# Performance work log

Measured on AMD Instinct MI355X. Metric: run time of the kernel, lower is better.

The kernel has to match this reference:

```python
import jax, jax.numpy as jnp
import numpy as np
import math

B, S, HD, NH, L, FF = 8, 512, 768, 12, 12, 3072
DH = HD // NH
EPS = 1e-12
REL_BINS, MAX_REL = 32, 128
REL2D_BINS, MAX_REL2D = 64, 256


def rel_bucket(rel_pos, num_buckets, max_distance):
    # bidirectional bucketing, faithful to relative_position_bucket
    nb = num_buckets // 2
    ret = (rel_pos > 0).astype(jnp.int32) * nb
    n = jnp.abs(rel_pos).astype(jnp.int32)
    max_exact = nb // 2
    is_small = n < max_exact
    scale = (nb - max_exact) / math.log(max_distance / max_exact)
    val = max_exact + (jnp.log(jnp.maximum(n, 1).astype(jnp.float32) / max_exact) * scale).astype(jnp.int32)
    val = jnp.minimum(val, nb - 1)
    return ret + jnp.where(is_small, n, val)


def layernorm(x, g, b):
    m = jnp.mean(x, axis=-1, keepdims=True)
    v = jnp.var(x, axis=-1, keepdims=True)
    return (x - m) * jax.lax.rsqrt(v + EPS) * g + b


def setup_inputs() -> dict:
    key = jax.random.key(0)
    ks = jax.random.split(key, 12)
    r = lambda k, shape: jax.random.normal(k, shape, jnp.float32) * 0.02
    z = lambda shape: jnp.zeros(shape, jnp.float32)
    o = lambda shape: jnp.ones(shape, jnp.float32)
    return {
        'hidden_states': jax.random.normal(ks[0], (B, S, HD), jnp.float32),
        'attention_mask': jnp.zeros((B, 1, 1, S), jnp.bool_),  # True = masked
        'position_ids': jnp.broadcast_to(jnp.arange(S, dtype=jnp.int32), (B, S)),
        'bbox': jax.random.randint(ks[1], (B, S, 4), 0, 1000, dtype=jnp.int32),
        'qkv_w': r(ks[2], (L, HD, 3 * HD)),
        'q_bias': z((L, HD)), 'v_bias': z((L, HD)),
        'attn_out_w': r(ks[3], (L, HD, HD)), 'attn_out_b': z((L, HD)),
        'ln1_g': o((L, HD)), 'ln1_b': z((L, HD)),
        'inter_w': r(ks[4], (L, HD, FF)), 'inter_b': z((L, FF)),
        'out_w': r(ks[5], (L, FF, HD)), 'out_b': z((L, HD)),
        'ln2_g': o((L, HD)), 'ln2_b': z((L, HD)),
        'rel_pos_w': r(ks[6], (REL_BINS, NH)),
        'rel_x_w': r(ks[7], (REL2D_BINS, NH)),
        'rel_y_w': r(ks[8], (REL2D_BINS, NH)),
    }


def reference(hidden_states, attention_mask, position_ids, bbox,
              qkv_w, q_bias, v_bias, attn_out_w, attn_out_b, ln1_g, ln1_b,
              inter_w, inter_b, out_w, out_b, ln2_g, ln2_b,
              rel_pos_w, rel_x_w, rel_y_w):
    # ---- 1D relative position bias: [B, NH, S, S] ----
    rp = position_ids[:, None, :] - position_ids[:, :, None]  # mem - query
    rel_pos = rel_pos_w[rel_bucket(rp, REL_BINS, MAX_REL)]     # [B,S,S,NH]
    rel_pos = rel_pos.transpose(0, 3, 1, 2)
    # ---- 2D spatial bias from bbox x (col 0) and y (col 3) ----
    px, py = bbox[:, :, 0], bbox[:, :, 3]
    bx = rel_bucket(px[:, None, :] - px[:, :, None], REL2D_BINS, MAX_REL2D)
    by = rel_bucket(py[:, None, :] - py[:, :, None], REL2D_BINS, MAX_REL2D)
    rel_2d = (rel_x_w[bx] + rel_y_w[by]).transpose(0, 3, 1, 2)  # [B,NH,S,S]
    bias = rel_pos + rel_2d
    mask = attention_mask.astype(jnp.bool_)  # [B,1,1,S], True = masked
    inv_sqrt_dh = 1.0 / math.sqrt(DH)

    def heads(x):  # [B,S,HD] -> [B,NH,S,DH]
        return x.reshape(B, S, NH, DH).transpose(0, 2, 1, 3)

    def layer(h, p):
        qw, qb, vb, aow, aob, g1, b1, iw, ib, ow, ob, g2, b2 = p
        qkv = h @ qw  # fast_qkv, no bias on the fused linear
        q, k, v = jnp.split(qkv, 3, axis=-1)
        q = heads(q + qb) * inv_sqrt_dh
        k = heads(k)
        v = heads(v + vb)
        scores = jnp.einsum('bhsd,bhtd->bhst', q, k) + bias
        scores = jnp.where(mask, -jnp.inf, scores.astype(jnp.float32))
        probs = jax.nn.softmax(scores, axis=-1).astype(h.dtype)
        ctx = jnp.einsum('bhst,bhtd->bhsd', probs, v)
        ctx = ctx.transpose(0, 2, 1, 3).reshape(B, S, HD)
        attn = layernorm(ctx @ aow + aob + h, g1, b1)
        ffn = jax.nn.gelu(attn @ iw + ib, approximate=False)
        out = layernorm(ffn @ ow + ob + attn, g2, b2)
        return out, None

    params = (qkv_w, q_bias, v_bias, attn_out_w, attn_out_b, ln1_g, ln1_b,
              inter_w, inter_b, out_w, out_b, ln2_g, ln2_b)
    h, _ = jax.lax.scan(layer, hidden_states, params)
    return h
```

## Files before the change

### kernel.cpp

```cpp
#include <hip/hip_runtime.h>
#include <math.h>

typedef unsigned short u16;
typedef short bf16x8 __attribute__((ext_vector_type(8)));
typedef unsigned short u16x8 __attribute__((ext_vector_type(8)));
typedef float f32x4 __attribute__((ext_vector_type(4)));

#define L_  12
#define B_  8
#define S_  512
#define HD_ 768
#define NH_ 12
#define DH_ 64
#define FF_ 3072

__device__ __forceinline__ u16 f2bf(float f) {
    unsigned u = __float_as_uint(f);
    u += 0x7fffu + ((u >> 16) & 1u);
    return (u16)(u >> 16);
}
__device__ __forceinline__ float bf2f(u16 h) {
    return __uint_as_float(((unsigned)h) << 16);
}

__device__ __forceinline__ void ld_lds16(const u16* g, u16* l) {
    __builtin_amdgcn_global_load_lds((const __attribute__((address_space(1))) void*)g,
                                     (__attribute__((address_space(3))) void*)l, 16, 0, 0);
}

__device__ __forceinline__ int rel_bucket(int rel, int num_buckets, int max_distance) {
    int nb = num_buckets >> 1;
    int ret = (rel > 0) ? nb : 0;
    int n = abs(rel);
    int max_exact = nb >> 1;
    if (n < max_exact) return ret + n;
    float scale = (float)(nb - max_exact) / logf((float)max_distance / (float)max_exact);
    int val = max_exact + (int)(logf(fmaxf((float)n, 1.0f) / (float)max_exact) * scale);
    val = min(val, nb - 1);
    return ret + val;
}

__global__ __launch_bounds__(256) void transpose_k(const float* __restrict__ in,
                                                   u16* __restrict__ out, int K, int N) {
    __shared__ u16 tile[32][33];
    const int k0 = blockIdx.x * 32, n0 = blockIdx.y * 32;
    const int tx = threadIdx.x & 31, ty = threadIdx.x >> 5;
#pragma unroll
    for (int r = 0; r < 32; r += 8)
        tile[ty + r][tx] = f2bf(in[(long)(k0 + ty + r) * N + n0 + tx]);
    __syncthreads();
#pragma unroll
    for (int r = 0; r < 32; r += 8)
        out[(long)(n0 + ty + r) * K + k0 + tx] = tile[tx][ty + r];
}

__global__ __launch_bounds__(256) void bucket_k(const int* __restrict__ pos,
                                                const int* __restrict__ bbox,
                                                unsigned* __restrict__ out) {
    const int bi = blockIdx.x;
    const int b = bi >> 9;
    const int t = threadIdx.x;
    const int pos_i = pos[bi];
    const int px_i = bbox[bi * 4 + 0];
    const int py_i = bbox[bi * 4 + 3];
    for (int j = t; j < S_; j += 256) {
        int bp = rel_bucket(pos[b * S_ + j] - pos_i, 32, 128);
        int bx = rel_bucket(bbox[(b * S_ + j) * 4 + 0] - px_i, 64, 256);
        int by = rel_bucket(bbox[(b * S_ + j) * 4 + 3] - py_i, 64, 256);
        out[((long)bi << 9) + j] = (unsigned)bp | ((unsigned)bx << 8) | ((unsigned)by << 16);
    }
}

__global__ __launch_bounds__(256) void init_k(const float* __restrict__ hs,
                                              float* __restrict__ h, u16* __restrict__ hb) {
    const int i = blockIdx.x * 256 + threadIdx.x;
    float v = hs[i];
    h[i] = v;
    hb[i] = f2bf(v);
}

template <int EPI>
__global__ __launch_bounds__(256) void gemm128_k(
    const u16* __restrict__ A, const u16* __restrict__ Bt, int N, int K, int Kc,
    long zStride,
    const float* __restrict__ bias, const float* __restrict__ bias2,
    float* __restrict__ outF,
    u16* __restrict__ oB0, u16* __restrict__ oB1, u16* __restrict__ oB2) {
    __shared__ __align__(16) u16 As[128 * 32];
    __shared__ __align__(16) u16 Bs[128 * 32];
    const int tid = threadIdx.x;
    const int wave = tid >> 6, lane = tid & 63;
    const int lrow = lane & 15, quad = lane >> 4;
    const int wr = wave >> 1, wc = wave & 1;
    const long zoff = (long)blockIdx.z * Kc;
    const u16* Ag = A + (long)blockIdx.x * 128 * K + (long)(tid >> 2) * K + ((tid & 3) << 3) + zoff;
    const u16* Bg = Bt + (long)blockIdx.y * 128 * K + (long)(tid >> 2) * K + ((tid & 3) << 3) + zoff;
    const long rs64 = (long)64 * K;
    u16* Al = As + tid * 8;
    u16* Bl = Bs + tid * 8;
    f32x4 acc[4][4] = {};
    for (int k0 = 0; k0 < Kc; k0 += 32) {
        ld_lds16(Ag + k0, Al);
        ld_lds16(Ag + rs64 + k0, Al + 2048);
        ld_lds16(Bg + k0, Bl);
        ld_lds16(Bg + rs64 + k0, Bl + 2048);
        __syncthreads();
        bf16x8 a[4], b[4];
#pragma unroll
        for (int i = 0; i < 4; i++)
            a[i] = *(const bf16x8*)(As + (wr * 64 + i * 16 + lrow) * 32 + (quad << 3));
#pragma unroll
        for (int j = 0; j < 4; j++)
            b[j] = *(const bf16x8*)(Bs + (wc * 64 + j * 16 + lrow) * 32 + (quad << 3));
#pragma unroll
        for (int i = 0; i < 4; i++)
#pragma unroll
            for (int j = 0; j < 4; j++)
                acc[i][j] = __builtin_amdgcn_mfma_f32_16x16x32_bf16(a[i], b[j], acc[i][j], 0, 0, 0);
        __syncthreads();
    }
    const int rbase = blockIdx.x * 128 + wr * 64 + (quad << 2);
    const int cbase = blockIdx.y * 128 + wc * 64 + lrow;
    const bool addb = (blockIdx.z == 0);
#pragma unroll
    for (int i = 0; i < 4; i++) {
#pragma unroll
        for (int j = 0; j < 4; j++) {
            const int gc = cbase + j * 16;
#pragma unroll
            for (int r = 0; r < 4; r++) {
                const int gr = rbase + i * 16 + r;
                float v = acc[i][j][r];
                if (EPI == 0) {
                    if (addb) v += bias[gc];
                    outF[(long)blockIdx.z * zStride + (long)gr * N + gc] = v;
                } else if (EPI == 1) {
                    v += bias[gc];
                    v = 0.5f * v * (1.0f + erff(v * 0.70710678118654752f));
                    oB0[(long)gr * N + gc] = f2bf(v);
                } else {
                    int b = gr >> 9, s = gr & 511;
                    int part = gc / HD_;
                    int cm = gc - part * HD_;
                    int hh = cm >> 6, d = cm & 63;
                    long hb = (long)(b * NH_ + hh);
                    if (part == 0) {
                        float q = (v + bias[cm]) * 0.125f;
                        oB0[(hb * S_ + s) * DH_ + d] = f2bf(q);
                    } else if (part == 1) {
                        oB1[(hb * S_ + s) * DH_ + d] = f2bf(v);
                    } else {
                        oB2[(hb * DH_ + d) * S_ + s] = f2bf(v + bias2[cm]);
                    }
                }
            }
        }
    }
}

__global__ __launch_bounds__(256) void attn_fused_k(
    const u16* __restrict__ q, const u16* __restrict__ k, const u16* __restrict__ vt,
    const unsigned* __restrict__ bk,
    const float* __restrict__ rpw, const float* __restrict__ rxw,
    const float* __restrict__ ryw, u16* __restrict__ ctx) {
    __shared__ float tb[1920];
    __shared__ __align__(16) u16 P[32768];
    const int t = threadIdx.x;
    for (int i = t; i < 384; i += 256) tb[i] = rpw[i];
    for (int i = t; i < 768; i += 256) { tb[384 + i] = rxw[i]; tb[1152 + i] = ryw[i]; }
    const int wv = t >> 6, lane = t & 63;
    const int lrow = lane & 15, quad = lane >> 4;
    const int bh = blockIdx.y, b = bh / NH_, h = bh - b * NH_;
    const int qt = blockIdx.x;
    const int q0 = qt * 64 + wv * 16;
    const u16* qb = q + ((long)bh * S_ + q0 + lrow) * DH_ + (quad << 3);
    const u16* kb = k + ((long)bh * S_ + lrow) * DH_ + (quad << 3);
    bf16x8 aq0 = *(const bf16x8*)qb;
    bf16x8 aq1 = *(const bf16x8*)(qb + 32);
    __syncthreads();
    f32x4 acc[32];
#pragma unroll
    for (int ct = 0; ct < 32; ct++) {
        const u16* kp = kb + (long)(ct * 16) * DH_;
        bf16x8 b0 = *(const bf16x8*)kp;
        bf16x8 b1 = *(const bf16x8*)(kp + 32);
        f32x4 z = {0.f, 0.f, 0.f, 0.f};
        z = __builtin_amdgcn_mfma_f32_16x16x32_bf16(aq0, b0, z, 0, 0, 0);
        acc[ct] = __builtin_amdgcn_mfma_f32_16x16x32_bf16(aq1, b1, z, 0, 0, 0);
    }
    float mx[4] = {-1e30f, -1e30f, -1e30f, -1e30f};
    const unsigned* bkb = bk + ((long)(b * S_ + q0 + (quad << 2)) << 9) + lrow;
#pragma unroll
    for (int r = 0; r < 4; r++) {
        const unsigned* br = bkb + ((long)r << 9);
#pragma unroll
        for (int ct = 0; ct < 32; ct++) {
            unsigned kk = br[ct * 16];
            float bi = tb[(kk & 255) * 12 + h] + tb[384 + ((kk >> 8) & 255) * 12 + h]
                     + tb[1152 + ((kk >> 16) & 255) * 12 + h];
            float x = acc[ct][r] + bi;
            acc[ct][r] = x;
            mx[r] = fmaxf(mx[r], x);
        }
    }
#pragma unroll
    for (int r = 0; r < 4; r++)
#pragma unroll
        for (int o = 8; o > 0; o >>= 1) mx[r] = fmaxf(mx[r], __shfl_xor(mx[r], o));
    float sm[4] = {0.f, 0.f, 0.f, 0.f};
#pragma unroll
    for (int ct = 0; ct < 32; ct++) {
#pragma unroll
        for (int r = 0; r < 4; r++) {
            float e = __expf(acc[ct][r] - mx[r]);
            acc[ct][r] = e;
            sm[r] += e;
        }
    }
#pragma unroll
    for (int r = 0; r < 4; r++) {
#pragma unroll
        for (int o = 8; o > 0; o >>= 1) sm[r] += __shfl_xor(sm[r], o);
        sm[r] = 1.0f / sm[r];
    }
    const int prow_w = (wv << 4) + (quad << 2);
#pragma unroll
    for (int ct = 0; ct < 32; ct++) {
#pragma unroll
        for (int r = 0; r < 4; r++) {
            int row = prow_w + r;
            int col = ct * 16 + lrow;
            int off = (row << 10) + ((((col >> 3) ^ (row & 7)) << 4)) + ((col & 7) << 1);
            *(u16*)((char*)P + off) = f2bf(acc[ct][r] * sm[r]);
        }
    }
    __syncthreads();
    f32x4 o[4] = {};
    const u16* vb = vt + ((long)bh * DH_ + lrow) * S_ + (quad << 3);
    const int prow = (wv << 4) + lrow;
#pragma unroll
    for (int c = 0; c < 16; c++) {
        int col0 = c * 32 + (quad << 3);
        int aoff = (prow << 10) + ((((col0 >> 3) ^ (prow & 7)) << 4));
        bf16x8 ap = *(const bf16x8*)((char*)P + aoff);
#pragma unroll
        for (int dt = 0; dt < 4; dt++) {
            bf16x8 bv = *(const bf16x8*)(vb + (long)(dt * 16) * S_ + c * 32);
            o[dt] = __builtin_amdgcn_mfma_f32_16x16x32_bf16(ap, bv, o[dt], 0, 0, 0);
        }
    }
    u16* cb = ctx + ((long)(b * S_ + qt * 64 + (wv << 4) + (quad << 2))) * HD_ + h * DH_ + lrow;
#pragma unroll
    for (int dt = 0; dt < 4; dt++)
#pragma unroll
        for (int i = 0; i < 4; i++)
            cb[(long)i * HD_ + dt * 16] = f2bf(o[dt][i]);
}

__global__ __launch_bounds__(256) void ln_k(const float* __restrict__ x0,
                                            const float* __restrict__ x1,
                                            const float* __restrict__ res,
                                            const float* __restrict__ g,
                                            const float* __restrict__ b,
                                            float* __restrict__ outF,
                                            u16* __restrict__ outB) {
    const long row = blockIdx.x;
    const float* xr = x0 + row * HD_;
    const float* yr = x1 + row * HD_;
    const float* rr = res + row * HD_;
    const int t = threadIdx.x;
    float v0 = xr[t] + yr[t] + rr[t];
    float v1 = xr[t + 256] + yr[t + 256] + rr[t + 256];
    float v2 = xr[t + 512] + yr[t + 512] + rr[t + 512];
    __shared__ float red[256];
    red[t] = v0 + v1 + v2;
    __syncthreads();
    for (int o = 128; o > 0; o >>= 1) {
        if (t < o) red[t] += red[t + o];
        __syncthreads();
    }
    float mean = red[0] * (1.0f / 768.0f);
    __syncthreads();
    float d0 = v0 - mean, d1 = v1 - mean, d2 = v2 - mean;
    red[t] = d0 * d0 + d1 * d1 + d2 * d2;
    __syncthreads();
    for (int o = 128; o > 0; o >>= 1) {
        if (t < o) red[t] += red[t + o];
        __syncthreads();
    }
    float rstd = rsqrtf(red[0] * (1.0f / 768.0f) + 1e-12f);
    float y0 = d0 * rstd * g[t] + b[t];
    float y1 = d1 * rstd * g[t + 256] + b[t + 256];
    float y2 = d2 * rstd * g[t + 512] + b[t + 512];
    outF[row * HD_ + t] = y0;
    outF[row * HD_ + t + 256] = y1;
    outF[row * HD_ + t + 512] = y2;
    outB[row * HD_ + t] = f2bf(y0);
    outB[row * HD_ + t + 256] = f2bf(y1);
    outB[row * HD_ + t + 512] = f2bf(y2);
}

extern "C" void kernel_launch(void* const* d_in, const int* in_sizes, int n_in,
                              void* d_out, int out_size, void* d_ws, size_t ws_size,
                              hipStream_t stream) {
    const float* hs     = (const float*)d_in[0];
    const int*   pos    = (const int*)d_in[2];
    const int*   bbox   = (const int*)d_in[3];
    const float* qkv_w  = (const float*)d_in[4];
    const float* q_bias = (const float*)d_in[5];
    const float* v_bias = (const float*)d_in[6];
    const float* aow    = (const float*)d_in[7];
    const float* aob    = (const float*)d_in[8];
    const float* g1     = (const float*)d_in[9];
    const float* b1     = (const float*)d_in[10];
    const float* iw     = (const float*)d_in[11];
    const float* ib     = (const float*)d_in[12];
    const float* ow     = (const float*)d_in[13];
    const float* ob     = (const float*)d_in[14];
    const float* g2     = (const float*)d_in[15];
    const float* b2     = (const float*)d_in[16];
    const float* rpw    = (const float*)d_in[17];
    const float* rxw    = (const float*)d_in[18];
    const float* ryw    = (const float*)d_in[19];

    char* wp = (char*)d_ws;
    auto take = [&](size_t bytes) -> char* {
        char* p = wp;
        wp += (bytes + 255) & ~(size_t)255;
        return p;
    };
    u16*   wq     = (u16*)take((size_t)2304 * 768 * 2);
    u16*   wa     = (u16*)take((size_t)768 * 768 * 2);
    u16*   wiT    = (u16*)take((size_t)3072 * 768 * 2);
    u16*   woT    = (u16*)take((size_t)768 * 3072 * 2);
    unsigned* buckets = (unsigned*)take((size_t)B_ * S_ * S_ * 4);
    char*  regA   = take((size_t)B_ * NH_ * S_ * S_ * 2);
    float* tmpF   = (float*)regA;
    float* tmpF2  = (float*)(regA + (size_t)B_ * S_ * HD_ * 4);
    u16*   ffnb   = (u16*)(regA + (size_t)2 * B_ * S_ * HD_ * 4);
    u16*   qbuf   = (u16*)take((size_t)B_ * NH_ * S_ * DH_ * 2);
    u16*   kbuf   = (u16*)take((size_t)B_ * NH_ * S_ * DH_ * 2);
    u16*   vtbuf  = (u16*)take((size_t)B_ * NH_ * S_ * DH_ * 2);
    u16*   hbf    = (u16*)take((size_t)B_ * S_ * HD_ * 2);
    u16*   ctxb   = (u16*)take((size_t)B_ * S_ * HD_ * 2);
    float* attnF  = (float*)take((size_t)B_ * S_ * HD_ * 4);
    u16*   attnB  = (u16*)take((size_t)B_ * S_ * HD_ * 2);

    if ((size_t)(wp - (char*)d_ws) > ws_size) return;

    dim3 blk(256);
    float* hout = (float*)d_out;
    const long ZS = (long)4096 * 768;

    bucket_k<<<dim3(B_ * S_), blk, 0, stream>>>(pos, bbox, buckets);
    init_k<<<dim3((B_ * S_ * HD_) / 256), blk, 0, stream>>>(hs, hout, hbf);

    for (int l = 0; l < L_; l++) {
        transpose_k<<<dim3(24, 72), blk, 0, stream>>>(qkv_w + (size_t)l * 768 * 2304, wq, 768, 2304);
        transpose_k<<<dim3(24, 24), blk, 0, stream>>>(aow + (size_t)l * 768 * 768, wa, 768, 768);
        transpose_k<<<dim3(24, 96), blk, 0, stream>>>(iw + (size_t)l * 768 * 3072, wiT, 768, 3072);
        transpose_k<<<dim3(96, 24), blk, 0, stream>>>(ow + (size_t)l * 3072 * 768, woT, 3072, 768);

        gemm128_k<2><<<dim3(32, 18, 1), blk, 0, stream>>>(
            hbf, wq, 2304, 768, 768, 0L, q_bias + l * HD_, v_bias + l * HD_,
            nullptr, qbuf, kbuf, vtbuf);

        attn_fused_k<<<dim3(8, 96), blk, 0, stream>>>(qbuf, kbuf, vtbuf, buckets,
                                                      rpw, rxw, ryw, ctxb);

        gemm128_k<0><<<dim3(32, 6, 2), blk, 0, stream>>>(
            ctxb, wa, 768, 768, 384, ZS, aob + l * HD_, nullptr,
            tmpF, nullptr, nullptr, nullptr);

        ln_k<<<dim3(B_ * S_), blk, 0, stream>>>(tmpF, tmpF2, hout,
                                                g1 + l * HD_, b1 + l * HD_, attnF, attnB);

        gemm128_k<1><<<dim3(32, 24, 1), blk, 0, stream>>>(
            attnB, wiT, 3072, 768, 768, 0L, ib + l * FF_, nullptr,
            nullptr, ffnb, nullptr, nullptr);

        gemm128_k<0><<<dim3(32, 6, 2), blk, 0, stream>>>(
            ffnb, woT, 768, 3072, 1536, ZS, ob + l * HD_, nullptr,
            tmpF, nullptr, nullptr, nullptr);

        ln_k<<<dim3(B_ * S_), blk, 0, stream>>>(tmpF, tmpF2, attnF,
                                                g2 + l * HD_, b2 + l * HD_, hout, hbf);
    }
}
```

Before: 3.676 ms.

## Precompute bf16 relative-position bias once and restructure attention P staging

Adds a bias_k kernel that expands bucket indices into a per-head bf16 bias tensor once, before the layer loop, so each layer's attention reads bias directly instead of doing three LDS table lookups per score. The attention kernel now computes K·Q (transposed) so each lane holds one query row, which simplifies the max and sum reductions to two shuffles. It also replaces the 64KB shared P buffer with small per-wave 4KB chunks processed in four column slices, with launch_bounds(256,3) to raise occupancy. The cost is an extra ~50MB workspace buffer and higher memory traffic for reading bf16 bias in every layer, with a fallback path when the workspace is too small.

```diff
diff --git a/kernel.cpp b/kernel.cpp
--- a/kernel.cpp
+++ b/kernel.cpp
@@ -68,6 +68,28 @@
         int bx = rel_bucket(bbox[(b * S_ + j) * 4 + 0] - px_i, 64, 256);
         int by = rel_bucket(bbox[(b * S_ + j) * 4 + 3] - py_i, 64, 256);
         out[((long)bi << 9) + j] = (unsigned)bp | ((unsigned)bx << 8) | ((unsigned)by << 16);
+    }
+}
+
+__global__ __launch_bounds__(256) void bias_k(const unsigned* __restrict__ bk,
+                                              const float* __restrict__ rpw,
+                                              const float* __restrict__ rxw,
+                                              const float* __restrict__ ryw,
+                                              u16* __restrict__ out) {
+    __shared__ float tb[1920];
+    const int t = threadIdx.x;
+    for (int i = t; i < 384; i += 256) tb[i] = rpw[i];
+    for (int i = t; i < 768; i += 256) { tb[384 + i] = rxw[i]; tb[1152 + i] = ryw[i]; }
+    __syncthreads();
+    const int bi = blockIdx.x;
+    const int b = bi >> 9, i = bi & 511;
+    const unsigned* br = bk + ((long)bi << 9);
+    for (int idx = t; idx < NH_ * S_; idx += 256) {
+        const int h = idx >> 9, j = idx & 511;
+        unsigned kk = br[j];
+        float v = tb[(kk & 255) * 12 + h] + tb[384 + ((kk >> 8) & 255) * 12 + h] +
+                  tb[1152 + ((kk >> 16) & 255) * 12 + h];
+        out[((long)(b * NH_ + h) * S_ + i) * S_ + j] = f2bf(v);
     }
 }
 
@@ -158,16 +180,19 @@
     }
 }
 
-__global__ __launch_bounds__(256) void attn_fused_k(
+template <bool USEB>
+__global__ __launch_bounds__(256, 3) void attn_fused_k(
     const u16* __restrict__ q, const u16* __restrict__ k, const u16* __restrict__ vt,
-    const unsigned* __restrict__ bk,
+    const u16* __restrict__ bias, const unsigned* __restrict__ bk,
     const float* __restrict__ rpw, const float* __restrict__ rxw,
     const float* __restrict__ ryw, u16* __restrict__ ctx) {
     __shared__ float tb[1920];
-    __shared__ __align__(16) u16 P[32768];
+    __shared__ __align__(16) u16 Pw[4][2048];
     const int t = threadIdx.x;
-    for (int i = t; i < 384; i += 256) tb[i] = rpw[i];
-    for (int i = t; i < 768; i += 256) { tb[384 + i] = rxw[i]; tb[1152 + i] = ryw[i]; }
+    if constexpr (!USEB) {
+        for (int i = t; i < 384; i += 256) tb[i] = rpw[i];
+        for (int i = t; i < 768; i += 256) { tb[384 + i] = rxw[i]; tb[1152 + i] = ryw[i]; }
+    }
     const int wv = t >> 6, lane = t & 63;
     const int lrow = lane & 15, quad = lane >> 4;
     const int bh = blockIdx.y, b = bh / NH_, h = bh - b * NH_;
@@ -175,81 +200,97 @@
     const int q0 = qt * 64 + wv * 16;
     const u16* qb = q + ((long)bh * S_ + q0 + lrow) * DH_ + (quad << 3);
     const u16* kb = k + ((long)bh * S_ + lrow) * DH_ + (quad << 3);
-    bf16x8 aq0 = *(const bf16x8*)qb;
-    bf16x8 aq1 = *(const bf16x8*)(qb + 32);
-    __syncthreads();
+    bf16x8 qf0 = *(const bf16x8*)qb;
+    bf16x8 qf1 = *(const bf16x8*)(qb + 32);
+    if constexpr (!USEB) __syncthreads();
     f32x4 acc[32];
 #pragma unroll
     for (int ct = 0; ct < 32; ct++) {
         const u16* kp = kb + (long)(ct * 16) * DH_;
-        bf16x8 b0 = *(const bf16x8*)kp;
-        bf16x8 b1 = *(const bf16x8*)(kp + 32);
+        bf16x8 k0 = *(const bf16x8*)kp;
+        bf16x8 k1 = *(const bf16x8*)(kp + 32);
         f32x4 z = {0.f, 0.f, 0.f, 0.f};
-        z = __builtin_amdgcn_mfma_f32_16x16x32_bf16(aq0, b0, z, 0, 0, 0);
-        acc[ct] = __builtin_amdgcn_mfma_f32_16x16x32_bf16(aq1, b1, z, 0, 0, 0);
-    }
-    float mx[4] = {-1e30f, -1e30f, -1e30f, -1e30f};
-    const unsigned* bkb = bk + ((long)(b * S_ + q0 + (quad << 2)) << 9) + lrow;
-#pragma unroll
-    for (int r = 0; r < 4; r++) {
-        const unsigned* br = bkb + ((long)r << 9);
+        z = __builtin_amdgcn_mfma_f32_16x16x32_bf16(k0, qf0, z, 0, 0, 0);
+        acc[ct] = __builtin_amdgcn_mfma_f32_16x16x32_bf16(k1, qf1, z, 0, 0, 0);
+    }
+    float m = -1e30f;
+    if constexpr (USEB) {
+        const u16* bb = bias + ((long)bh * S_ + q0 + lrow) * S_ + (quad << 2);
 #pragma unroll
         for (int ct = 0; ct < 32; ct++) {
-            unsigned kk = br[ct * 16];
-            float bi = tb[(kk & 255) * 12 + h] + tb[384 + ((kk >> 8) & 255) * 12 + h]
-                     + tb[1152 + ((kk >> 16) & 255) * 12 + h];
-            float x = acc[ct][r] + bi;
-            acc[ct][r] = x;
-            mx[r] = fmaxf(mx[r], x);
-        }
-    }
-#pragma unroll
-    for (int r = 0; r < 4; r++)
-#pragma unroll
-        for (int o = 8; o > 0; o >>= 1) mx[r] = fmaxf(mx[r], __shfl_xor(mx[r], o));
-    float sm[4] = {0.f, 0.f, 0.f, 0.f};
+            ushort4 b4 = *(const ushort4*)(bb + ct * 16);
+            acc[ct][0] += bf2f(b4.x);
+            acc[ct][1] += bf2f(b4.y);
+            acc[ct][2] += bf2f(b4.z);
+            acc[ct][3] += bf2f(b4.w);
+            m = fmaxf(m, fmaxf(fmaxf(acc[ct][0], acc[ct][1]), fmaxf(acc[ct][2], acc[ct][3])));
+        }
+    } else {
+        const unsigned* br = bk + ((long)(b * S_ + q0 + lrow) << 9) + (quad << 2);
+#pragma unroll
+        for (int ct = 0; ct < 32; ct++) {
+            uint4 k4 = *(const uint4*)(br + ct * 16);
+            unsigned ka[4] = {k4.x, k4.y, k4.z, k4.w};
+#pragma unroll
+            for (int r = 0; r < 4; r++) {
+                unsigned kk = ka[r];
+                acc[ct][r] += tb[(kk & 255) * 12 + h] + tb[384 + ((kk >> 8) & 255) * 12 + h] +
+                              tb[1152 + ((kk >> 16) & 255) * 12 + h];
+            }
+            m = fmaxf(m, fmaxf(fmaxf(acc[ct][0], acc[ct][1]), fmaxf(acc[ct][2], acc[ct][3])));
+        }
+    }
+    m = fmaxf(m, __shfl_xor(m, 16));
+    m = fmaxf(m, __shfl_xor(m, 32));
+    float s = 0.f;
 #pragma unroll
     for (int ct = 0; ct < 32; ct++) {
 #pragma unroll
         for (int r = 0; r < 4; r++) {
-            float e = __expf(acc[ct][r] - mx[r]);
+            float e = __expf(acc[ct][r] - m);
             acc[ct][r] = e;
-            sm[r] += e;
-        }
-    }
-#pragma unroll
-    for (int r = 0; r < 4; r++) {
-#pragma unroll
-        for (int o = 8; o > 0; o >>= 1) sm[r] += __shfl_xor(sm[r], o);
-        sm[r] = 1.0f / sm[r];
-    }
-    const int prow_w = (wv << 4) + (quad << 2);
-#pragma unroll
-    for (int ct = 0; ct < 32; ct++) {
-#pragma unroll
-        for (int r = 0; r < 4; r++) {
-            int row = prow_w + r;
-            int col = ct * 16 + lrow;
-            int off = (row << 10) + ((((col >> 3) ^ (row & 7)) << 4)) + ((col & 7) << 1);
-            *(u16*)((char*)P + off) = f2bf(acc[ct][r] * sm[r]);
-        }
-    }
-    __syncthreads();
+            s += e;
+        }
+    }
+    s += __shfl_xor(s, 16);
+    s += __shfl_xor(s, 32);
+    const float inv = 1.0f / s;
     f32x4 o[4] = {};
     const u16* vb = vt + ((long)bh * DH_ + lrow) * S_ + (quad << 3);
-    const int prow = (wv << 4) + lrow;
-#pragma unroll
-    for (int c = 0; c < 16; c++) {
-        int col0 = c * 32 + (quad << 3);
-        int aoff = (prow << 10) + ((((col0 >> 3) ^ (prow & 7)) << 4));
-        bf16x8 ap = *(const bf16x8*)((char*)P + aoff);
-#pragma unroll
-        for (int dt = 0; dt < 4; dt++) {
-            bf16x8 bv = *(const bf16x8*)(vb + (long)(dt * 16) * S_ + c * 32);
-            o[dt] = __builtin_amdgcn_mfma_f32_16x16x32_bf16(ap, bv, o[dt], 0, 0, 0);
-        }
-    }
-    u16* cb = ctx + ((long)(b * S_ + qt * 64 + (wv << 4) + (quad << 2))) * HD_ + h * DH_ + lrow;
+    u16* pw = &Pw[wv][0];
+    const int wg = quad >> 1;
+    const int wbyte = (quad & 1) << 3;
+    const int rsw = lrow & 7;
+#pragma unroll
+    for (int c = 0; c < 4; c++) {
+        asm volatile("s_waitcnt lgkmcnt(0)" ::: "memory");
+        __builtin_amdgcn_sched_barrier(0);
+#pragma unroll
+        for (int lc = 0; lc < 8; lc++) {
+            const f32x4 a = acc[c * 8 + lc];
+            ushort4 pk;
+            pk.x = f2bf(a[0] * inv);
+            pk.y = f2bf(a[1] * inv);
+            pk.z = f2bf(a[2] * inv);
+            pk.w = f2bf(a[3] * inv);
+            const int g = lc * 2 + wg;
+            *(ushort4*)((char*)pw + lrow * 256 + (((g ^ rsw)) << 4) + wbyte) = pk;
+        }
+        asm volatile("s_waitcnt lgkmcnt(0)" ::: "memory");
+        __builtin_amdgcn_sched_barrier(0);
+#pragma unroll
+        for (int ss = 0; ss < 4; ss++) {
+            bf16x8 ap = *(const bf16x8*)((char*)pw + lrow * 256 +
+                                         ((((ss << 2) + quad) ^ rsw) << 4));
+            const u16* vp = vb + c * 128 + ss * 32;
+#pragma unroll
+            for (int dt = 0; dt < 4; dt++) {
+                bf16x8 bv = *(const bf16x8*)(vp + (long)(dt * 16) * S_);
+                o[dt] = __builtin_amdgcn_mfma_f32_16x16x32_bf16(ap, bv, o[dt], 0, 0, 0);
+            }
+        }
+    }
+    u16* cb = ctx + ((long)(b * S_ + qt * 64 + wv * 16 + (quad << 2))) * HD_ + h * DH_ + lrow;
 #pragma unroll
     for (int dt = 0; dt < 4; dt++)
 #pragma unroll
@@ -345,8 +386,11 @@
     u16*   ctxb   = (u16*)take((size_t)B_ * S_ * HD_ * 2);
     float* attnF  = (float*)take((size_t)B_ * S_ * HD_ * 4);
     u16*   attnB  = (u16*)take((size_t)B_ * S_ * HD_ * 2);
-
-    if ((size_t)(wp - (char*)d_ws) > ws_size) return;
+    char*  base_end = wp;
+    u16*   biasT  = (u16*)take((size_t)B_ * NH_ * S_ * S_ * 2);
+
+    if ((size_t)(base_end - (char*)d_ws) > ws_size) return;
+    const bool useBias = (size_t)(wp - (char*)d_ws) <= ws_size;
 
     dim3 blk(256);
     float* hout = (float*)d_out;
@@ -354,6 +398,8 @@
 
     bucket_k<<<dim3(B_ * S_), blk, 0, stream>>>(pos, bbox, buckets);
     init_k<<<dim3((B_ * S_ * HD_) / 256), blk, 0, stream>>>(hs, hout, hbf);
+    if (useBias)
+        bias_k<<<dim3(B_ * S_), blk, 0, stream>>>(buckets, rpw, rxw, ryw, biasT);
 
     for (int l = 0; l < L_; l++) {
         transpose_k<<<dim3(24, 72), blk, 0, stream>>>(qkv_w + (size_t)l * 768 * 2304, wq, 768, 2304);
@@ -365,8 +411,12 @@
             hbf, wq, 2304, 768, 768, 0L, q_bias + l * HD_, v_bias + l * HD_,
             nullptr, qbuf, kbuf, vtbuf);
 
-        attn_fused_k<<<dim3(8, 96), blk, 0, stream>>>(qbuf, kbuf, vtbuf, buckets,
-                                                      rpw, rxw, ryw, ctxb);
+        if (useBias)
+            attn_fused_k<true><<<dim3(8, 96), blk, 0, stream>>>(
+                qbuf, kbuf, vtbuf, biasT, buckets, rpw, rxw, ryw, ctxb);
+        else
+            attn_fused_k<false><<<dim3(8, 96), blk, 0, stream>>>(
+                qbuf, kbuf, vtbuf, nullptr, buckets, rpw, rxw, ryw, ctxb);
 
         gemm128_k<0><<<dim3(32, 6, 2), blk, 0, stream>>>(
             ctxb, wa, 768, 768, 384, ZS, aob + l * HD_, nullptr,
```

Result: faster. 3.385 ms (-7.9%).
